# Optimization experiments

Hardware: AMD Instinct MI355X
Metric: run time of the kernel (lower is better)

The kernel has to match this reference:

```python
import jax, jax.numpy as jnp
import numpy as np


def setup_inputs() -> dict:
    key0 = jax.random.key(0)
    kq, kk, kv = jax.random.split(key0, 3)
    B, H, L, S, D = 2, 8, 2048, 2048, 64
    query = jax.random.normal(kq, (B, H, L, D), dtype=jnp.float32)
    key = jax.random.normal(kk, (B, H, S, D), dtype=jnp.float32)
    value = jax.random.normal(kv, (B, H, S, D), dtype=jnp.float32)
    return {"query": query, "key": key, "value": value}


def reference(query, key, value):
    # Original computes matmul(q[b,h,l,1,d,1], k[b,h,1,s,1,d]) -> [B,H,L,S,D,D]
    # outer products, divides by sqrt(query.shape[-1]) AFTER unsqueeze (==1, no-op),
    # then sums dims (4,5). That is algebraically exactly rowsum(q)*rowsum(k).
    qsum = query.sum(axis=-1)                       # [B,H,L]
    ksum = key.sum(axis=-1)                         # [B,H,S]
    score = qsum[..., :, None] * ksum[..., None, :]  # [B,H,L,S]
    attn = jax.nn.softmax(score, axis=-1)            # softmax over S
    out = jnp.einsum('bhls,bhsd->bhld', attn, value)  # [B,H,L,D]
    return out
```

## Files before the change

kernel.cpp:

```cpp
#include <hip/hip_runtime.h>
#include <hip/hip_bf16.h>

#define BH 16
#define L 2048
#define S 2048
#define DD 64
#define BM 64
#define BK 64
#define LDSPAD 8
#define LDW (BK + LDSPAD)

typedef __attribute__((ext_vector_type(4))) float f32x4;
typedef __bf16 bf16x8 __attribute__((ext_vector_type(8)));

union FragU {
  bf16x8 f;
  __hip_bfloat162 h2[4];
};

#define MFMA16(a, b, c) __builtin_amdgcn_mfma_f32_16x16x32_bf16((a), (b), (c), 0, 0, 0)

__device__ inline __hip_bfloat162 exp2pk(float al2, float nsl2, float k0,
                                         float k1) {
  float e0 = __builtin_amdgcn_exp2f(fmaf(al2, k0, nsl2));
  float e1 = __builtin_amdgcn_exp2f(fmaf(al2, k1, nsl2));
  return __float22bfloat162_rn(make_float2(e0, e1));
}

__global__ __launch_bounds__(256) void prep_kernel(
    const float* __restrict__ k, const float* __restrict__ v,
    float* __restrict__ ks, __hip_bfloat16* __restrict__ vt) {
  __shared__ __hip_bfloat16 tile[DD][LDW];
  int t = threadIdx.x;
  if (blockIdx.x < 2048) {
    int g = blockIdx.x * 256 + t;
    int row = g >> 4;
    int l16 = g & 15;
    float4 x = reinterpret_cast<const float4*>(k + (size_t)row * DD)[l16];
    float s = x.x + x.y + x.z + x.w;
    s += __shfl_xor(s, 1);
    s += __shfl_xor(s, 2);
    s += __shfl_xor(s, 4);
    s += __shfl_xor(s, 8);
    if (l16 == 0) ks[row] = s;
  } else {
    int bid = blockIdx.x - 2048;
    int s0 = (bid & 31) * 64;
    int bh = bid >> 5;
    int srow = t >> 4;
    int d4 = (t & 15) * 4;
#pragma unroll
    for (int kk = 0; kk < 4; ++kk) {
      int s = srow + kk * 16;
      float4 val = *reinterpret_cast<const float4*>(
          v + ((size_t)(bh * S + s0 + s)) * DD + d4);
      tile[d4 + 0][s] = __float2bfloat16(val.x);
      tile[d4 + 1][s] = __float2bfloat16(val.y);
      tile[d4 + 2][s] = __float2bfloat16(val.z);
      tile[d4 + 3][s] = __float2bfloat16(val.w);
    }
    __syncthreads();
    int dd = t >> 3;
    int j = t & 7;
#pragma unroll
    for (int kk = 0; kk < 2; ++kk) {
      int d = dd + kk * 32;
      uint4 val = *reinterpret_cast<const uint4*>(&tile[d][j * 8]);
      *reinterpret_cast<uint4*>(vt + ((size_t)(bh * DD + d)) * S + s0 + j * 8) =
          val;
    }
  }
}

__global__ __launch_bounds__(512, 4) void attn_kernel(
    const float* __restrict__ q, const __hip_bfloat16* __restrict__ vt,
    const float* __restrict__ ks, float* __restrict__ out) {
  int l0 = blockIdx.x * BM;
  int bh = blockIdx.y;

  __shared__ char smem[2 * 4 * DD * LDW * 2] __attribute__((aligned(16)));
  __shared__ float a_row[BM];
  __shared__ float red[16];
  __shared__ float drow[4][2][2][16];

  auto ldsVT = reinterpret_cast<__hip_bfloat16(*)[4][DD][LDW]>(smem);
  auto cmb = reinterpret_cast<float(*)[32][65]>(smem);

  int t = threadIdx.x;
  int lane = t & 63;
  int w = t >> 6;
  int rg = w >> 2;
  int sg = w & 3;
  int m = lane & 15;
  int qd = lane >> 4;

  const __hip_bfloat16* vtb = vt + (size_t)bh * DD * S;
  const float* ksb = ks + (size_t)bh * S;

  int tg = t >> 7;
  int u = t & 127;
  int vd = u >> 1;
  int vh = u & 1;

  const __hip_bfloat16* vs0 =
      vtb + (size_t)vd * S + tg * 64 + vh * 32;
  uint4 p0 = reinterpret_cast<const uint4*>(vs0)[0];
  uint4 p1 = reinterpret_cast<const uint4*>(vs0)[1];
  uint4 p2 = reinterpret_cast<const uint4*>(vs0)[2];
  uint4 p3 = reinterpret_cast<const uint4*>(vs0)[3];
  int kb0 = sg * 64;
  float4 kA0 = *reinterpret_cast<const float4*>(ksb + kb0 + qd * 8);
  float4 kA1 = *reinterpret_cast<const float4*>(ksb + kb0 + qd * 8 + 4);
  float4 kB0 = *reinterpret_cast<const float4*>(ksb + kb0 + 32 + qd * 8);
  float4 kB1 = *reinterpret_cast<const float4*>(ksb + kb0 + 32 + qd * 8 + 4);

  {
    int r = t >> 3;
    int p = t & 7;
    const float* qp = q + ((size_t)(bh * L + l0 + r)) * DD + p * 8;
    float4 x0 = reinterpret_cast<const float4*>(qp)[0];
    float4 x1 = reinterpret_cast<const float4*>(qp)[1];
    float s = (x0.x + x0.y + x0.z + x0.w) + (x1.x + x1.y + x1.z + x1.w);
    s += __shfl_xor(s, 1);
    s += __shfl_xor(s, 2);
    s += __shfl_xor(s, 4);
    if (p == 0) a_row[r] = s;
  }

  {
    float4 y = *reinterpret_cast<const float4*>(ksb + t * 4);
    float mx = fmaxf(fmaxf(y.x, y.y), fmaxf(y.z, y.w));
    float mn = fminf(fminf(y.x, y.y), fminf(y.z, y.w));
#pragma unroll
    for (int off = 1; off < 64; off <<= 1) {
      mx = fmaxf(mx, __shfl_xor(mx, off));
      mn = fminf(mn, __shfl_xor(mn, off));
    }
    if (lane == 0) {
      red[w] = mx;
      red[8 + w] = mn;
    }
  }

  {
    uint4* dst = reinterpret_cast<uint4*>(&ldsVT[0][tg][vd][vh * 32]);
    dst[0] = p0;
    dst[1] = p1;
    dst[2] = p2;
    dst[3] = p3;
  }
  __syncthreads();

  float kmax = red[0], kmin = red[8];
#pragma unroll
  for (int i = 1; i < 8; ++i) {
    kmax = fmaxf(kmax, red[i]);
    kmin = fminf(kmin, red[8 + i]);
  }
  const float LOG2E = 1.44269504088896f;
  float ar0 = a_row[rg * 32 + m];
  float ar1 = a_row[rg * 32 + 16 + m];
  float al2_0 = ar0 * LOG2E, al2_1 = ar1 * LOG2E;
  float nsl2_0 = -al2_0 * ((ar0 > 0.f) ? kmax : kmin);
  float nsl2_1 = -al2_1 * ((ar1 > 0.f) ? kmax : kmin);

  FragU of;
  {
    __hip_bfloat162 one2 = __float22bfloat162_rn(make_float2(1.f, 1.f));
    of.h2[0] = of.h2[1] = of.h2[2] = of.h2[3] = one2;
  }

  f32x4 acc0[4], acc1[4];
  f32x4 ad0 = (f32x4){0.f, 0.f, 0.f, 0.f};
  f32x4 ad1 = (f32x4){0.f, 0.f, 0.f, 0.f};
#pragma unroll
  for (int c = 0; c < 4; ++c) {
    acc0[c] = (f32x4){0.f, 0.f, 0.f, 0.f};
    acc1[c] = (f32x4){0.f, 0.f, 0.f, 0.f};
  }

  for (int step = 0; step < 8; ++step) {
    int buf = step & 1;

    int sn = (step < 7) ? step + 1 : 7;
    const __hip_bfloat16* vs =
        vtb + (size_t)vd * S + (sn * 4 + tg) * 64 + vh * 32;
    uint4 n0 = reinterpret_cast<const uint4*>(vs)[0];
    uint4 n1 = reinterpret_cast<const uint4*>(vs)[1];
    uint4 n2 = reinterpret_cast<const uint4*>(vs)[2];
    uint4 n3 = reinterpret_cast<const uint4*>(vs)[3];

    FragU fA0, fA1, fB0, fB1;
    fA0.h2[0] = exp2pk(al2_0, nsl2_0, kA0.x, kA0.y);
    fA0.h2[1] = exp2pk(al2_0, nsl2_0, kA0.z, kA0.w);
    fA0.h2[2] = exp2pk(al2_0, nsl2_0, kA1.x, kA1.y);
    fA0.h2[3] = exp2pk(al2_0, nsl2_0, kA1.z, kA1.w);
    fA1.h2[0] = exp2pk(al2_0, nsl2_0, kB0.x, kB0.y);
    fA1.h2[1] = exp2pk(al2_0, nsl2_0, kB0.z, kB0.w);
    fA1.h2[2] = exp2pk(al2_0, nsl2_0, kB1.x, kB1.y);
    fA1.h2[3] = exp2pk(al2_0, nsl2_0, kB1.z, kB1.w);
    fB0.h2[0] = exp2pk(al2_1, nsl2_1, kA0.x, kA0.y);
    fB0.h2[1] = exp2pk(al2_1, nsl2_1, kA0.z, kA0.w);
    fB0.h2[2] = exp2pk(al2_1, nsl2_1, kA1.x, kA1.y);
    fB0.h2[3] = exp2pk(al2_1, nsl2_1, kA1.z, kA1.w);
    fB1.h2[0] = exp2pk(al2_1, nsl2_1, kB0.x, kB0.y);
    fB1.h2[1] = exp2pk(al2_1, nsl2_1, kB0.z, kB0.w);
    fB1.h2[2] = exp2pk(al2_1, nsl2_1, kB1.x, kB1.y);
    fB1.h2[3] = exp2pk(al2_1, nsl2_1, kB1.z, kB1.w);

    int kbn = ((step < 7) ? (step + 1) * 4 + sg : 28 + sg) * 64;
    kA0 = *reinterpret_cast<const float4*>(ksb + kbn + qd * 8);
    kA1 = *reinterpret_cast<const float4*>(ksb + kbn + qd * 8 + 4);
    kB0 = *reinterpret_cast<const float4*>(ksb + kbn + 32 + qd * 8);
    kB1 = *reinterpret_cast<const float4*>(ksb + kbn + 32 + qd * 8 + 4);

    ad0 = MFMA16(fA0.f, of.f, ad0);
    ad0 = MFMA16(fA1.f, of.f, ad0);
    ad1 = MFMA16(fB0.f, of.f, ad1);
    ad1 = MFMA16(fB1.f, of.f, ad1);

#pragma unroll
    for (int c = 0; c < 4; ++c) {
      uint4 b0 =
          *reinterpret_cast<const uint4*>(&ldsVT[buf][sg][c * 16 + m][qd * 8]);
      bf16x8 bb0 = __builtin_bit_cast(bf16x8, b0);
      acc0[c] = MFMA16(fA0.f, bb0, acc0[c]);
      acc1[c] = MFMA16(fB0.f, bb0, acc1[c]);
      uint4 b1 = *reinterpret_cast<const uint4*>(
          &ldsVT[buf][sg][c * 16 + m][32 + qd * 8]);
      bf16x8 bb1 = __builtin_bit_cast(bf16x8, b1);
      acc0[c] = MFMA16(fA1.f, bb1, acc0[c]);
      acc1[c] = MFMA16(fB1.f, bb1, acc1[c]);
    }

    if (step < 7) {
      uint4* dst =
          reinterpret_cast<uint4*>(&ldsVT[(step + 1) & 1][tg][vd][vh * 32]);
      dst[0] = n0;
      dst[1] = n1;
      dst[2] = n2;
      dst[3] = n3;
      __syncthreads();
    }
  }

  if (m == 0) {
#pragma unroll
    for (int i = 0; i < 4; ++i) {
      drow[sg][rg][0][qd * 4 + i] = ad0[i];
      drow[sg][rg][1][qd * 4 + i] = ad1[i];
    }
  }
  if (sg >= 2) {
    int z = rg * 2 + (sg - 2);
#pragma unroll
    for (int c = 0; c < 4; ++c)
#pragma unroll
      for (int i = 0; i < 4; ++i) {
        cmb[z][qd * 4 + i][c * 16 + m] = acc0[c][i];
        cmb[z][16 + qd * 4 + i][c * 16 + m] = acc1[c][i];
      }
  }
  __syncthreads();
  if (sg < 2) {
    int z = rg * 2 + sg;
#pragma unroll
    for (int c = 0; c < 4; ++c)
#pragma unroll
      for (int i = 0; i < 4; ++i) {
        acc0[c][i] += cmb[z][qd * 4 + i][c * 16 + m];
        acc1[c][i] += cmb[z][16 + qd * 4 + i][c * 16 + m];
      }
  }
  if (sg == 1) {
    int z = rg * 2 + 1;
#pragma unroll
    for (int c = 0; c < 4; ++c)
#pragma unroll
      for (int i = 0; i < 4; ++i) {
        cmb[z][qd * 4 + i][c * 16 + m] = acc0[c][i];
        cmb[z][16 + qd * 4 + i][c * 16 + m] = acc1[c][i];
      }
  }
  __syncthreads();
  if (sg == 0) {
    int z = rg * 2 + 1;
    float inv0[4], inv1[4];
#pragma unroll
    for (int i = 0; i < 4; ++i) {
      int r = qd * 4 + i;
      inv0[i] = 1.0f / (drow[0][rg][0][r] + drow[1][rg][0][r] +
                        drow[2][rg][0][r] + drow[3][rg][0][r]);
      inv1[i] = 1.0f / (drow[0][rg][1][r] + drow[1][rg][1][r] +
                        drow[2][rg][1][r] + drow[3][rg][1][r]);
    }
    float* ob = out + ((size_t)(bh * L + l0 + rg * 32)) * DD;
#pragma unroll
    for (int c = 0; c < 4; ++c)
#pragma unroll
      for (int i = 0; i < 4; ++i) {
        float t0 = acc0[c][i] + cmb[z][qd * 4 + i][c * 16 + m];
        float t1 = acc1[c][i] + cmb[z][16 + qd * 4 + i][c * 16 + m];
        ob[(size_t)(qd * 4 + i) * DD + c * 16 + m] = t0 * inv0[i];
        ob[(size_t)(16 + qd * 4 + i) * DD + c * 16 + m] = t1 * inv1[i];
      }
  }
}

extern "C" void kernel_launch(void* const* d_in, const int* in_sizes, int n_in,
                              void* d_out, int out_size, void* d_ws,
                              size_t ws_size, hipStream_t stream) {
  const float* q = (const float*)d_in[0];
  const float* k = (const float*)d_in[1];
  const float* v = (const float*)d_in[2];
  float* out = (float*)d_out;
  float* ws = (float*)d_ws;

  float* ks = ws;
  __hip_bfloat16* vt = (__hip_bfloat16*)(ws + BH * S);

  prep_kernel<<<2048 + 512, 256, 0, stream>>>(k, v, ks, vt);
  attn_kernel<<<dim3(L / BM, BH), 512, 0, stream>>>(q, vt, ks, out);
}
```

Before: 93.90 us.

## Stage V tiles via direct global-to-LDS loads with XOR-swizzled layout

Replaces the register-staged prefetch of the transposed V tiles (global load into registers, then an LDS store) with global_load_lds direct-to-LDS transfers. The LDS layout moves from padded rows to an XOR-swizzled unpadded layout to avoid bank conflicts, and the combine buffer gets a rotated layout. This frees registers and removes the LDS store instructions, but relies on the async LDS loads being complete at the existing barriers, which carry no explicit wait for them.

```diff
diff --git a/kernel.cpp b/kernel.cpp
--- a/kernel.cpp
+++ b/kernel.cpp
@@ -12,6 +12,7 @@
 
 typedef __attribute__((ext_vector_type(4))) float f32x4;
 typedef __bf16 bf16x8 __attribute__((ext_vector_type(8)));
+typedef unsigned int u32;
 
 union FragU {
   bf16x8 f;
@@ -25,6 +26,12 @@
   float e0 = __builtin_amdgcn_exp2f(fmaf(al2, k0, nsl2));
   float e1 = __builtin_amdgcn_exp2f(fmaf(al2, k1, nsl2));
   return __float22bfloat162_rn(make_float2(e0, e1));
+}
+
+__device__ __forceinline__ void gload_lds16(const void* g, void* l) {
+  __builtin_amdgcn_global_load_lds(
+      (const __attribute__((address_space(1))) u32*)g,
+      (__attribute__((address_space(3))) u32*)l, 16, 0, 0);
 }
 
 __global__ __launch_bounds__(256) void prep_kernel(
@@ -78,13 +85,10 @@
   int l0 = blockIdx.x * BM;
   int bh = blockIdx.y;
 
-  __shared__ char smem[2 * 4 * DD * LDW * 2] __attribute__((aligned(16)));
+  __shared__ char smem[2 * 4 * 8192] __attribute__((aligned(16)));
   __shared__ float a_row[BM];
   __shared__ float red[16];
   __shared__ float drow[4][2][2][16];
-
-  auto ldsVT = reinterpret_cast<__hip_bfloat16(*)[4][DD][LDW]>(smem);
-  auto cmb = reinterpret_cast<float(*)[32][65]>(smem);
 
   int t = threadIdx.x;
   int lane = t & 63;
@@ -96,18 +100,26 @@
 
   const __hip_bfloat16* vtb = vt + (size_t)bh * DD * S;
   const float* ksb = ks + (size_t)bh * S;
-
-  int tg = t >> 7;
-  int u = t & 127;
-  int vd = u >> 1;
-  int vh = u & 1;
-
-  const __hip_bfloat16* vs0 =
-      vtb + (size_t)vd * S + tg * 64 + vh * 32;
-  uint4 p0 = reinterpret_cast<const uint4*>(vs0)[0];
-  uint4 p1 = reinterpret_cast<const uint4*>(vs0)[1];
-  uint4 p2 = reinterpret_cast<const uint4*>(vs0)[2];
-  uint4 p3 = reinterpret_cast<const uint4*>(vs0)[3];
+  const char* vtbc = (const char*)vtb;
+
+  const size_t laneg =
+      (size_t)(lane >> 3) * (S * 2) + (size_t)(((lane & 7) ^ (lane >> 3)) << 4);
+  const size_t wrowg = (size_t)((w & 1) * 32) * (S * 2);
+  char* lwbase = smem + w * 4096;
+
+#define STAGE(g, b)                                                         \
+  {                                                                         \
+    const char* gb0 =                                                       \
+        vtbc + (size_t)(((g)*4 + (w >> 1)) * 64) * 2 + wrowg + laneg;       \
+    char* lb0 = lwbase + (b)*32768;                                         \
+    gload_lds16(gb0, lb0);                                                  \
+    gload_lds16(gb0 + (size_t)8 * S * 2, lb0 + 1024);                       \
+    gload_lds16(gb0 + (size_t)16 * S * 2, lb0 + 2048);                      \
+    gload_lds16(gb0 + (size_t)24 * S * 2, lb0 + 3072);                      \
+  }
+
+  STAGE(0, 0);
+
   int kb0 = sg * 64;
   float4 kA0 = *reinterpret_cast<const float4*>(ksb + kb0 + qd * 8);
   float4 kA1 = *reinterpret_cast<const float4*>(ksb + kb0 + qd * 8 + 4);
@@ -141,14 +153,6 @@
       red[8 + w] = mn;
     }
   }
-
-  {
-    uint4* dst = reinterpret_cast<uint4*>(&ldsVT[0][tg][vd][vh * 32]);
-    dst[0] = p0;
-    dst[1] = p1;
-    dst[2] = p2;
-    dst[3] = p3;
-  }
   __syncthreads();
 
   float kmax = red[0], kmin = red[8];
@@ -179,16 +183,12 @@
     acc1[c] = (f32x4){0.f, 0.f, 0.f, 0.f};
   }
 
+  const int sw0 = (qd ^ (m & 7)) << 4;
+
   for (int step = 0; step < 8; ++step) {
     int buf = step & 1;
 
-    int sn = (step < 7) ? step + 1 : 7;
-    const __hip_bfloat16* vs =
-        vtb + (size_t)vd * S + (sn * 4 + tg) * 64 + vh * 32;
-    uint4 n0 = reinterpret_cast<const uint4*>(vs)[0];
-    uint4 n1 = reinterpret_cast<const uint4*>(vs)[1];
-    uint4 n2 = reinterpret_cast<const uint4*>(vs)[2];
-    uint4 n3 = reinterpret_cast<const uint4*>(vs)[3];
+    if (step < 7) STAGE(step + 1, buf ^ 1);
 
     FragU fA0, fA1, fB0, fB1;
     fA0.h2[0] = exp2pk(al2_0, nsl2_0, kA0.x, kA0.y);
@@ -219,29 +219,21 @@
     ad1 = MFMA16(fB0.f, of.f, ad1);
     ad1 = MFMA16(fB1.f, of.f, ad1);
 
+    const char* rb = smem + buf * 32768 + sg * 8192;
 #pragma unroll
     for (int c = 0; c < 4; ++c) {
-      uint4 b0 =
-          *reinterpret_cast<const uint4*>(&ldsVT[buf][sg][c * 16 + m][qd * 8]);
+      const char* rowp = rb + (c * 16 + m) * 128;
+      uint4 b0 = *reinterpret_cast<const uint4*>(rowp + sw0);
       bf16x8 bb0 = __builtin_bit_cast(bf16x8, b0);
       acc0[c] = MFMA16(fA0.f, bb0, acc0[c]);
       acc1[c] = MFMA16(fB0.f, bb0, acc1[c]);
-      uint4 b1 = *reinterpret_cast<const uint4*>(
-          &ldsVT[buf][sg][c * 16 + m][32 + qd * 8]);
+      uint4 b1 = *reinterpret_cast<const uint4*>(rowp + (sw0 ^ 64));
       bf16x8 bb1 = __builtin_bit_cast(bf16x8, b1);
       acc0[c] = MFMA16(fA1.f, bb1, acc0[c]);
       acc1[c] = MFMA16(fB1.f, bb1, acc1[c]);
     }
 
-    if (step < 7) {
-      uint4* dst =
-          reinterpret_cast<uint4*>(&ldsVT[(step + 1) & 1][tg][vd][vh * 32]);
-      dst[0] = n0;
-      dst[1] = n1;
-      dst[2] = n2;
-      dst[3] = n3;
-      __syncthreads();
-    }
+    if (step < 7) __syncthreads();
   }
 
   if (m == 0) {
@@ -251,14 +243,19 @@
       drow[sg][rg][1][qd * 4 + i] = ad1[i];
     }
   }
+
+  auto cmb = [&](int z, int r, int col) -> float* {
+    return reinterpret_cast<float*>(smem + z * 8192) + r * 64 +
+           ((col + r * 4) & 63);
+  };
   if (sg >= 2) {
     int z = rg * 2 + (sg - 2);
 #pragma unroll
     for (int c = 0; c < 4; ++c)
 #pragma unroll
       for (int i = 0; i < 4; ++i) {
-        cmb[z][qd * 4 + i][c * 16 + m] = acc0[c][i];
-        cmb[z][16 + qd * 4 + i][c * 16 + m] = acc1[c][i];
+        *cmb(z, qd * 4 + i, c * 16 + m) = acc0[c][i];
+        *cmb(z, 16 + qd * 4 + i, c * 16 + m) = acc1[c][i];
       }
   }
   __syncthreads();
@@ -268,8 +265,8 @@
     for (int c = 0; c < 4; ++c)
 #pragma unroll
       for (int i = 0; i < 4; ++i) {
-        acc0[c][i] += cmb[z][qd * 4 + i][c * 16 + m];
-        acc1[c][i] += cmb[z][16 + qd * 4 + i][c * 16 + m];
+        acc0[c][i] += *cmb(z, qd * 4 + i, c * 16 + m);
+        acc1[c][i] += *cmb(z, 16 + qd * 4 + i, c * 16 + m);
       }
   }
   if (sg == 1) {
@@ -278,8 +275,8 @@
     for (int c = 0; c < 4; ++c)
 #pragma unroll
       for (int i = 0; i < 4; ++i) {
-        cmb[z][qd * 4 + i][c * 16 + m] = acc0[c][i];
-        cmb[z][16 + qd * 4 + i][c * 16 + m] = acc1[c][i];
+        *cmb(z, qd * 4 + i, c * 16 + m) = acc0[c][i];
+        *cmb(z, 16 + qd * 4 + i, c * 16 + m) = acc1[c][i];
       }
   }
   __syncthreads();
@@ -299,12 +296,13 @@
     for (int c = 0; c < 4; ++c)
 #pragma unroll
       for (int i = 0; i < 4; ++i) {
-        float t0 = acc0[c][i] + cmb[z][qd * 4 + i][c * 16 + m];
-        float t1 = acc1[c][i] + cmb[z][16 + qd * 4 + i][c * 16 + m];
+        float t0 = acc0[c][i] + *cmb(z, qd * 4 + i, c * 16 + m);
+        float t1 = acc1[c][i] + *cmb(z, 16 + qd * 4 + i, c * 16 + m);
         ob[(size_t)(qd * 4 + i) * DD + c * 16 + m] = t0 * inv0[i];
         ob[(size_t)(16 + qd * 4 + i) * DD + c * 16 + m] = t1 * inv1[i];
       }
   }
+#undef STAGE
 }
 
 extern "C" void kernel_launch(void* const* d_in, const int* in_sizes, int n_in,
```

Result: no change. 93.42 us (-0.5%).
